# Optimization experiments

Hardware: AMD Instinct MI355X
Metric: run time of the kernel (lower is better)

The kernel has to match this reference:

```python
import jax, jax.numpy as jnp
import numpy as np
from jax import lax

B, S, E, H, V, L = 16, 256, 256, 256, 50000, 9


def setup_inputs() -> dict:
    key = jax.random.key(0)
    ks = jax.random.split(key, 12)
    s = 0.05
    return {
        "input_ids": jax.random.randint(ks[0], (B, S), 0, V),
        "attention_mask": jnp.ones((B, S), dtype=jnp.int32),
        "labels": jax.random.randint(ks[1], (B, S), 0, L),
        "embedding": jax.random.normal(ks[2], (V, E), jnp.float32) * s,
        "w_ih_l0": jax.random.normal(ks[3], (2, 4 * H, E), jnp.float32) * s,
        "w_ih_rest": jax.random.normal(ks[4], (3, 2, 4 * H, 2 * H), jnp.float32) * s,
        "w_hh": jax.random.normal(ks[5], (4, 2, 4 * H, H), jnp.float32) * s,
        "b": jax.random.normal(ks[6], (4, 2, 2, 4 * H), jnp.float32) * s,
        "ln_g": jnp.ones((2 * H,), jnp.float32),
        "ln_b": jnp.zeros((2 * H,), jnp.float32),
        "lin_w": jax.random.normal(ks[7], (L, 2 * H), jnp.float32) * s,
        "lin_b": jnp.zeros((L,), jnp.float32),
        "crf_start": jax.random.normal(ks[8], (L,), jnp.float32) * s,
        "crf_end": jax.random.normal(ks[9], (L,), jnp.float32) * s,
        "crf_trans": jax.random.normal(ks[10], (L, L), jnp.float32) * s,
    }


def _lstm_dir(x, w_ih, w_hh, b_ih, b_hh, reverse):
    # x: [B,S,in]; PyTorch gate order i,f,g,o packed along 4H.
    Bb = x.shape[0]
    Hh = w_hh.shape[1]
    xg = jnp.einsum('bsi,gi->bsg', x, w_ih) + b_ih + b_hh  # precompute input projection
    if reverse:
        xg = xg[:, ::-1]

    def step(carry, g):
        h, c = carry
        g = g + h @ w_hh.T
        i, f, gg, o = jnp.split(g, 4, axis=-1)
        c = jax.nn.sigmoid(f) * c + jax.nn.sigmoid(i) * jnp.tanh(gg)
        h = jax.nn.sigmoid(o) * jnp.tanh(c)
        return (h, c), h

    z = jnp.zeros((Bb, Hh), x.dtype)
    _, hs = lax.scan(step, (z, z), jnp.swapaxes(xg, 0, 1))
    hs = jnp.swapaxes(hs, 0, 1)  # [B,S,H]
    if reverse:
        hs = hs[:, ::-1]
    return hs


def _forward(input_ids, attention_mask, labels, embedding, w_ih_l0, w_ih_rest,
             w_hh, b, ln_g, ln_b, lin_w, lin_b, crf_start, crf_end, crf_trans):
    x = embedding[input_ids]  # [B,S,E]
    for layer in range(4):
        wf = w_ih_l0[0] if layer == 0 else w_ih_rest[layer - 1, 0]
        wb = w_ih_l0[1] if layer == 0 else w_ih_rest[layer - 1, 1]
        hf = _lstm_dir(x, wf, w_hh[layer, 0], b[layer, 0, 0], b[layer, 0, 1], False)
        hb = _lstm_dir(x, wb, w_hh[layer, 1], b[layer, 1, 0], b[layer, 1, 1], True)
        x = jnp.concatenate([hf, hb], axis=-1)  # [B,S,2H]
    # dropout is identity in eval mode
    mu = x.mean(-1, keepdims=True)
    var = ((x - mu) ** 2).mean(-1, keepdims=True)
    x = (x - mu) * lax.rsqrt(var + 1e-5) * ln_g + ln_b
    logits = jnp.einsum('bsh,lh->bsl', x, lin_w) + lin_b  # emissions [B,S,L]

    # CRF negative log-likelihood (torchcrf semantics, reduction='sum')
    Bb = logits.shape[0]
    mask_f = attention_mask.astype(logits.dtype)
    bidx = jnp.arange(Bb)
    first = labels[:, 0]
    num = crf_start[first] + logits[bidx, 0, first]
    em_t = jnp.swapaxes(logits, 0, 1)[1:]  # [S-1,B,L]
    tprev = labels[:, :-1].T
    tcur = labels[:, 1:].T
    mt = mask_f[:, 1:].T

    def num_step(s, inp):
        e, tp, tc, m = inp
        return s + (crf_trans[tp, tc] + e[bidx, tc]) * m, None

    num, _ = lax.scan(num_step, num, (em_t, tprev, tcur, mt))
    last = jnp.sum(attention_mask, axis=1).astype(jnp.int32) - 1
    num = num + crf_end[labels[bidx, last]]

    alpha = crf_start + logits[:, 0]  # [B,L]

    def den_step(a, inp):
        e, m = inp
        nxt = jax.nn.logsumexp(a[:, :, None] + crf_trans[None] + e[:, None, :], axis=1)
        return jnp.where(m[:, None] > 0, nxt, a), None

    alpha, _ = lax.scan(den_step, alpha, (em_t, mt))
    denom = jax.nn.logsumexp(alpha + crf_end, axis=-1)
    loss = -(num - denom).sum()
    return logits, loss


def reference(input_ids, attention_mask, labels, embedding, w_ih_l0, w_ih_rest,
              w_hh, b, ln_g, ln_b, lin_w, lin_b, crf_start, crf_end, crf_trans):
    return _forward(input_ids, attention_mask, labels, embedding, w_ih_l0,
                    w_ih_rest, w_hh, b, ln_g, ln_b, lin_w, lin_b,
                    crf_start, crf_end, crf_trans)
```

## Files before the change

### kernel.cpp

```cpp
#include <hip/hip_runtime.h>
#include <math.h>
#include <stdint.h>

#define BB 16
#define SS 256
#define LL 9
#define ROWS 4096
#define HP 272

typedef __attribute__((ext_vector_type(8))) short short8;
typedef __attribute__((ext_vector_type(4))) float f32x4;
typedef __attribute__((ext_vector_type(8))) int i32x8;

#define HSCALE 256.0f
#define LOG2E  1.44269504f
#define WCONST 1477.3199f
#define SCALE_ONE 0x7F7F7F7Fu
#define SCALE_IFO 0x6D6D6D6Du
#define SCALE_G   0x6E6E6E6Eu

__device__ __forceinline__ unsigned short f2bf(float f) {
  unsigned u = __float_as_uint(f);
  return (unsigned short)((u + 0x7FFF + ((u >> 16) & 1)) >> 16);
}
__device__ __forceinline__ float bf2f(unsigned short s) {
  return __uint_as_float(((unsigned)s) << 16);
}

__device__ __forceinline__ void gl2lds16(const void* g, void* l) {
  __builtin_amdgcn_global_load_lds(
      (const __attribute__((address_space(1))) void*)g,
      (__attribute__((address_space(3))) void*)l, 16, 0, 0);
}

__device__ __forceinline__ void barrier_lds_only() {
  asm volatile("s_waitcnt lgkmcnt(0)" ::: "memory");
  __builtin_amdgcn_s_barrier();
  asm volatile("" ::: "memory");
}

__global__ __launch_bounds__(256) void embed_bf16(
    const int* __restrict__ ids, const float* __restrict__ emb,
    unsigned short* __restrict__ x0) {
  int row = blockIdx.x;
  int id = ids[row];
  x0[(size_t)row * 256 + threadIdx.x] = f2bf(emb[(size_t)id * 256 + threadIdx.x]);
}

__global__ __launch_bounds__(64) void pack_whh_mx(
    const float* __restrict__ w, unsigned* __restrict__ wfrag) {
  int nb = blockIdx.x, ks2 = blockIdx.y, z = blockIdx.z;
  int lane = threadIdx.x, qq = lane >> 4, col = lane & 15;
  int g = nb >> 4;
  float csc = (g == 2) ? WCONST : -WCONST;
  const float* wp = w + (size_t)z * 1024 * 256 + (size_t)(nb * 16 + col) * 256 +
                    ks2 * 128 + qq * 32;
  unsigned* op = wfrag + (((size_t)(z * 64 + nb) * 2 + ks2) * 64 + lane) * 8;
#pragma unroll
  for (int u = 0; u < 8; ++u) {
    float v0 = wp[u * 4 + 0] * csc, v1 = wp[u * 4 + 1] * csc;
    float v2 = wp[u * 4 + 2] * csc, v3 = wp[u * 4 + 3] * csc;
    unsigned pk = __builtin_amdgcn_cvt_pk_fp8_f32(v0, v1, 0, false);
    pk = __builtin_amdgcn_cvt_pk_fp8_f32(v2, v3, pk, true);
    op[u] = pk;
  }
}

__global__ __launch_bounds__(256) void bias_perm(
    const float* __restrict__ b2, float* __restrict__ biasPF) {
  int i = blockIdx.x * 256 + threadIdx.x;
  int l = i >> 11, r = i & 2047;
  int dir = r >> 10, np = r & 1023;
  int n = ((np & 3) << 8) + (np >> 2);
  float cg = ((np & 3) == 2) ? (2.0f * LOG2E) : (-LOG2E);
  biasPF[i] = (b2[l * 4096 + dir * 2048 + n] + b2[l * 4096 + dir * 2048 + 1024 + n]) * cg;
}

__global__ __launch_bounds__(256) void prep_wih(
    const float* __restrict__ w_l0, const float* __restrict__ w_rest,
    unsigned short* __restrict__ wp, const long* __restrict__ woff_dummy) {
  int l = blockIdx.z;
  int Ksh = l ? 9 : 8;
  int K = 1 << Ksh;
  long total = (long)2 * 1024 * K;
  long idx = (long)blockIdx.x * 256 + threadIdx.x;
  if (idx >= total) return;
  int k = (int)(idx & (K - 1));
  long r = idx >> Ksh;
  int np = (int)(r & 1023), dir = (int)(r >> 10);
  int nph = ((np & 3) << 8) + (np >> 2);
  float cg = ((np & 3) == 2) ? (2.0f * LOG2E) : (-LOG2E);
  const float* src = l ? (w_rest + (size_t)(l - 1) * 2 * 1024 * 512) : w_l0;
  size_t off = l ? (524288 + (size_t)(l - 1) * 1048576) : 0;
  wp[off + idx] = f2bf(src[((size_t)dir * 1024 + nph) * K + k] * cg);
}

__global__ __launch_bounds__(512) void gemm_xg128(
    const unsigned short* __restrict__ A, int K,
    const unsigned short* __restrict__ BP,
    const float* __restrict__ biasPF,
    unsigned short* __restrict__ xgP) {
  int dir = blockIdx.z;
  int n0 = blockIdx.x * 128, m0 = blockIdx.y * 128;
  int tid = threadIdx.x;
  int wv = tid >> 6, lane = tid & 63, quad = lane >> 4, col = lane & 15;
  __shared__ unsigned short As[2][128 * 32];
  __shared__ unsigned short Bs[2][128 * 32];
  const unsigned short* Bw = BP + (size_t)dir * 1024 * K;

  int srow = lane >> 2;
  int scol = (lane & 3) * 8;
  const unsigned short* ga = A + (size_t)(m0 + wv * 16 + srow) * K + scol;
  const unsigned short* gb = Bw + (size_t)(n0 + wv * 16 + srow) * K + scol;
  int lofs = wv * 512;

  int wm = wv & 1;
  int wn = wv >> 1;
  f32x4 acc[4][2];
#pragma unroll
  for (int mt = 0; mt < 4; ++mt)
#pragma unroll
    for (int nt = 0; nt < 2; ++nt) acc[mt][nt] = (f32x4){0.f, 0.f, 0.f, 0.f};

  int nIter = K >> 5;
  gl2lds16(ga, &As[0][lofs]);
  gl2lds16(gb, &Bs[0][lofs]);
  ga += 32; gb += 32;
  __syncthreads();

  for (int it = 0; it < nIter; ++it) {
    int cb = it & 1;
    if (it + 1 < nIter) {
      gl2lds16(ga, &As[cb ^ 1][lofs]);
      gl2lds16(gb, &Bs[cb ^ 1][lofs]);
      ga += 32; gb += 32;
    }
    short8 bf0 = *(const short8*)&Bs[cb][(wn * 32 + col) * 32 + quad * 8];
    short8 bf1 = *(const short8*)&Bs[cb][(wn * 32 + 16 + col) * 32 + quad * 8];
#pragma unroll
    for (int mt = 0; mt < 4; ++mt) {
      short8 af = *(const short8*)&As[cb][(wm * 64 + mt * 16 + col) * 32 + quad * 8];
      acc[mt][0] = __builtin_amdgcn_mfma_f32_16x16x32_bf16(af, bf0, acc[mt][0], 0, 0, 0);
      acc[mt][1] = __builtin_amdgcn_mfma_f32_16x16x32_bf16(af, bf1, acc[mt][1], 0, 0, 0);
    }
    __syncthreads();
  }

#pragma unroll
  for (int nt = 0; nt < 2; ++nt) {
    int np = n0 + wn * 32 + nt * 16 + col;
    float bia = biasPF[dir * 1024 + np];
#pragma unroll
    for (int mt = 0; mt < 4; ++mt) {
#pragma unroll
      for (int r = 0; r < 4; ++r) {
        int row = m0 + wm * 64 + mt * 16 + quad * 4 + r;
        xgP[((size_t)dir * ROWS + row) * 1024 + np] = f2bf(acc[mt][nt][r] + bia);
      }
    }
  }
}

__global__ __launch_bounds__(1024, 4) void lstm_mx(
    const unsigned short* __restrict__ xgP,
    const unsigned* __restrict__ wfrag,
    unsigned short* __restrict__ xout) {
  int dir = blockIdx.x & 1;
  int bg = blockIdx.x >> 1;
  int tid = threadIdx.x;
  int wv = tid >> 6, lane = tid & 63;
  int quad = lane >> 4, col = lane & 15;

  __shared__ __align__(16) unsigned char Hfrag[2][4 * HP];

  {
    int* hz = (int*)&Hfrag[0][0];
    for (int i = tid; i < HP; i += 1024) hz[i] = 0;
  }

  i32x8 wf[4][2];
#pragma unroll
  for (int g = 0; g < 4; ++g) {
    int nb = g * 16 + wv;
#pragma unroll
    for (int ks2 = 0; ks2 < 2; ++ks2)
      wf[g][ks2] = *(const i32x8*)(wfrag +
          (((size_t)(dir * 64 + nb) * 2 + ks2) * 64 + lane) * 8);
  }

  int aoff = ((lane & 15) >> 2) * HP + (lane >> 4) * 32;

  int j = 16 * wv + col;
  int b = bg * 4 + quad;
  int pos0 = dir ? (SS - 1) : 0;
  int dstep = dir ? -1 : 1;
  const unsigned short* xq_ptr =
      xgP + ((size_t)dir * ROWS + (size_t)b * SS + pos0) * 1024 + j * 4;
  unsigned short* xo_ptr = xout + ((size_t)b * SS + pos0) * 512 + dir * 256 + j;
  int xq_d = dstep * 1024;
  int xo_d = dstep * 512;
  int hw = quad * HP + j;

  float Cp = 0.f;
  int cur = 0;
  ushort4 xq_n = *(const ushort4*)xq_ptr;
  xq_ptr += xq_d;
  __syncthreads();

  for (int t = 0; t < SS; ++t) {
    ushort4 xq = xq_n;
    xq_n = *(const ushort4*)xq_ptr;
    xq_ptr += xq_d;

    i32x8 af0 = *(const i32x8*)&Hfrag[cur][aoff];
    i32x8 af1 = *(const i32x8*)&Hfrag[cur][aoff + 128];

    f32x4 acc[4];
    acc[0] = (f32x4){bf2f(xq.x), 0.f, 0.f, 0.f};
    acc[1] = (f32x4){bf2f(xq.y), 0.f, 0.f, 0.f};
    acc[2] = (f32x4){bf2f(xq.z), 0.f, 0.f, 0.f};
    acc[3] = (f32x4){bf2f(xq.w), 0.f, 0.f, 0.f};
#pragma unroll
    for (int g = 0; g < 4; ++g) {
      unsigned sb = (g == 2) ? SCALE_G : SCALE_IFO;
      acc[g] = __builtin_amdgcn_mfma_scale_f32_16x16x128_f8f6f4(
          af0, wf[g][0], acc[g], 0, 0, 0, SCALE_ONE, 0, sb);
      acc[g] = __builtin_amdgcn_mfma_scale_f32_16x16x128_f8f6f4(
          af1, wf[g][1], acc[g], 0, 0, 0, SCALE_ONE, 0, sb);
    }

    int nxt = cur ^ 1;
    float gi = acc[0][0];
    float gf = acc[1][0];
    float gt = acc[2][0];
    float go = acc[3][0];
    float si = __builtin_amdgcn_rcpf(1.0f + __builtin_amdgcn_exp2f(gi));
    float sf = __builtin_amdgcn_rcpf(1.0f + __builtin_amdgcn_exp2f(gf));
    float so = __builtin_amdgcn_rcpf(1.0f + __builtin_amdgcn_exp2f(go));
    float rg = __builtin_amdgcn_rcpf(1.0f + __builtin_amdgcn_exp2f(gt));
    float tg2 = fmaf(-4.0f * LOG2E, rg, 2.0f * LOG2E);
    Cp = fmaf(sf, Cp, si * tg2);
    float rc = __builtin_amdgcn_rcpf(1.0f + __builtin_amdgcn_exp2f(Cp));
    float h = so * fmaf(-2.0f, rc, 1.0f);

    unsigned pk = __builtin_amdgcn_cvt_pk_fp8_f32(h * HSCALE, h * HSCALE, 0, false);
    Hfrag[nxt][hw] = (unsigned char)(pk & 0xFF);
    *xo_ptr = f2bf(h);
    xo_ptr += xo_d;

    barrier_lds_only();
    cur = nxt;
  }
}

__global__ __launch_bounds__(64) void ln_logits(
    const unsigned short* __restrict__ X, const float* __restrict__ g,
    const float* __restrict__ bt, const float* __restrict__ W,
    const float* __restrict__ lb, float* __restrict__ out) {
  int row = blockIdx.x;
  int lane = threadIdx.x;
  const unsigned short* x = X + (size_t)row * 512;
  float v[8];
  float s = 0.f, s2 = 0.f;
#pragma unroll
  for (int i = 0; i < 8; ++i) {
    v[i] = bf2f(x[lane + 64 * i]);
    s += v[i];
    s2 += v[i] * v[i];
  }
#pragma unroll
  for (int off = 32; off; off >>= 1) {
    s += __shfl_down(s, off, 64);
    s2 += __shfl_down(s2, off, 64);
  }
  s = __shfl(s, 0, 64);
  s2 = __shfl(s2, 0, 64);
  float mu = s * (1.f / 512.f);
  float var = s2 * (1.f / 512.f) - mu * mu;
  float rstd = rsqrtf(var + 1e-5f);
  float y[8];
#pragma unroll
  for (int i = 0; i < 8; ++i) {
    int e = lane + 64 * i;
    y[i] = (v[i] - mu) * rstd * g[e] + bt[e];
  }
  for (int l = 0; l < LL; ++l) {
    float p = 0.f;
#pragma unroll
    for (int i = 0; i < 8; ++i) p += y[i] * W[(size_t)l * 512 + lane + 64 * i];
#pragma unroll
    for (int off = 32; off; off >>= 1) p += __shfl_down(p, off, 64);
    if (lane == 0) out[(size_t)row * LL + l] = p + lb[l];
  }
}

__global__ __launch_bounds__(256) void crf_kernel(
    const float* __restrict__ logits, const int* __restrict__ labels,
    const int* __restrict__ mask, const float* __restrict__ cs,
    const float* __restrict__ ce, const float* __restrict__ ct,
    float* __restrict__ loss_out) {
  __shared__ float trans[9][12];
  __shared__ float alpha[2][BB][12];
  __shared__ float numsh[BB];
  __shared__ float res[BB];
  int tid = threadIdx.x;
  int b = tid >> 4;
  int i = tid & 15;
  if (tid < 81) trans[tid / 9][tid % 9] = ct[tid];
  __syncthreads();
  const float* lg = logits + (size_t)b * SS * LL;
  const int* lbp = labels + (size_t)b * SS;
  const int* mk = mask + (size_t)b * SS;

  float np = 0.f;
  int msum = 0;
  for (int t = i; t < SS; t += 16) {
    msum += mk[t];
    if (t == 0) {
      int l0 = lbp[0];
      np += cs[l0] + lg[l0];
    } else {
      float m = (float)mk[t];
      np += (trans[lbp[t - 1]][lbp[t]] + lg[(size_t)t * LL + lbp[t]]) * m;
    }
  }
#pragma unroll
  for (int off = 8; off; off >>= 1) {
    np += __shfl_down(np, off, 16);
    msum += __shfl_down(msum, off, 16);
  }
  if (i == 0) {
    int last = msum - 1;
    numsh[b] = np + ce[lbp[last]];
  }

  if (i < LL) alpha[0][b][i] = cs[i] + lg[i];
  int cur = 0;
  for (int t = 1; t < SS; ++t) {
    if (i < LL) {
      float e = lg[(size_t)t * LL + i];
      float av[9];
      float mmax = -1e30f;
#pragma unroll
      for (int p = 0; p < LL; ++p) {
        float vv = alpha[cur][b][p] + trans[p][i];
        av[p] = vv;
        mmax = fmaxf(mmax, vv);
      }
      float ssum = 0.f;
#pragma unroll
      for (int p = 0; p < LL; ++p) ssum += __expf(av[p] - mmax);
      float anew = e + mmax + logf(ssum);
      float aold = alpha[cur][b][i];
      alpha[cur ^ 1][b][i] = (mk[t] > 0) ? anew : aold;
    }
    cur ^= 1;
  }
  if (i == 0) {
    float arr[9];
    float m2 = -1e30f;
#pragma unroll
    for (int cc = 0; cc < LL; ++cc) {
      arr[cc] = alpha[cur][b][cc] + ce[cc];
      m2 = fmaxf(m2, arr[cc]);
    }
    float ssd = 0.f;
#pragma unroll
    for (int cc = 0; cc < LL; ++cc) ssd += __expf(arr[cc] - m2);
    float denom = m2 + logf(ssd);
    res[b] = numsh[b] - denom;
  }
  __syncthreads();
  if (tid == 0) {
    float Lsum = 0.f;
    for (int b2 = 0; b2 < BB; ++b2) Lsum += res[b2];
    loss_out[0] = -Lsum;
  }
}

extern "C" void kernel_launch(void* const* d_in, const int* in_sizes, int n_in,
                              void* d_out, int out_size, void* d_ws, size_t ws_size,
                              hipStream_t stream) {
  const int* input_ids = (const int*)d_in[0];
  const int* attn_mask = (const int*)d_in[1];
  const int* labels = (const int*)d_in[2];
  const float* embedding = (const float*)d_in[3];
  const float* w_ih_l0 = (const float*)d_in[4];
  const float* w_ih_rest = (const float*)d_in[5];
  const float* w_hh = (const float*)d_in[6];
  const float* bvec = (const float*)d_in[7];
  const float* ln_g = (const float*)d_in[8];
  const float* ln_b = (const float*)d_in[9];
  const float* lin_w = (const float*)d_in[10];
  const float* lin_b = (const float*)d_in[11];
  const float* crf_start = (const float*)d_in[12];
  const float* crf_end = (const float*)d_in[13];
  const float* crf_trans = (const float*)d_in[14];
  float* out = (float*)d_out;
  char* base = (char*)d_ws;

  unsigned short* x0    = (unsigned short*)(base);
  unsigned short* xoutA = (unsigned short*)(base + (2u << 20));
  unsigned short* xoutB = (unsigned short*)(base + (6u << 20));
  unsigned short* xgP   = (unsigned short*)(base + (10u << 20));
  unsigned*       wfrag = (unsigned*)(base + (26u << 20));
  float*          biasPF= (float*)(base + (28u << 20));
  unsigned short* wihP  = (unsigned short*)(base + (29u << 20));

  embed_bf16<<<ROWS, 256, 0, stream>>>(input_ids, embedding, x0);
  pack_whh_mx<<<dim3(64, 2, 8), 64, 0, stream>>>(w_hh, wfrag);
  bias_perm<<<32, 256, 0, stream>>>(bvec, biasPF);
  prep_wih<<<dim3(4096, 1, 4), 256, 0, stream>>>(w_ih_l0, w_ih_rest, wihP, nullptr);

  const size_t WOFF[4] = {0, 524288, 1572864, 2621440};

  const unsigned short* cur = x0;
  unsigned short* nxt = xoutA;
  for (int l = 0; l < 4; ++l) {
    int K = l ? 512 : 256;
    gemm_xg128<<<dim3(8, 32, 2), 512, 0, stream>>>(
        cur, K, wihP + WOFF[l], biasPF + (size_t)l * 2048, xgP);
    lstm_mx<<<8, 1024, 0, stream>>>(xgP, wfrag + (size_t)l * 131072, nxt);
    cur = nxt;
    nxt = (nxt == xoutA) ? xoutB : xoutA;
  }

  ln_logits<<<ROWS, 64, 0, stream>>>(cur, ln_g, ln_b, lin_w, lin_b, out);
  crf_kernel<<<1, 256, 0, stream>>>(out, labels, attn_mask, crf_start, crf_end,
                                    crf_trans, out + (size_t)ROWS * LL);
}
```

Before: 1.001 ms.

## Fuse prep kernels, stage GEMM epilogue through LDS, pack LN rows per block

Merges the four preprocessing kernels (embedding gather, W_ih pack, W_hh fp8 pack, bias permute) into one launch dispatched by block index, which removes three kernel launches. The xg GEMM epilogue now writes its tile into LDS and stores it to global memory as coalesced 16-byte vectors, replacing the scattered 2-byte stores. ln_logits handles four rows per 256-thread block instead of one row per 64-thread block. Total time is dominated by the sequential LSTM kernels, so these changes only trim launch and memory overhead around them.

```diff
diff --git a/kernel.cpp b/kernel.cpp
--- a/kernel.cpp
+++ b/kernel.cpp
@@ -39,60 +39,74 @@
   asm volatile("" ::: "memory");
 }
 
-__global__ __launch_bounds__(256) void embed_bf16(
+__global__ __launch_bounds__(256) void prep_all(
     const int* __restrict__ ids, const float* __restrict__ emb,
-    unsigned short* __restrict__ x0) {
-  int row = blockIdx.x;
-  int id = ids[row];
-  x0[(size_t)row * 256 + threadIdx.x] = f2bf(emb[(size_t)id * 256 + threadIdx.x]);
-}
-
-__global__ __launch_bounds__(64) void pack_whh_mx(
-    const float* __restrict__ w, unsigned* __restrict__ wfrag) {
-  int nb = blockIdx.x, ks2 = blockIdx.y, z = blockIdx.z;
-  int lane = threadIdx.x, qq = lane >> 4, col = lane & 15;
-  int g = nb >> 4;
-  float csc = (g == 2) ? WCONST : -WCONST;
-  const float* wp = w + (size_t)z * 1024 * 256 + (size_t)(nb * 16 + col) * 256 +
-                    ks2 * 128 + qq * 32;
-  unsigned* op = wfrag + (((size_t)(z * 64 + nb) * 2 + ks2) * 64 + lane) * 8;
-#pragma unroll
-  for (int u = 0; u < 8; ++u) {
-    float v0 = wp[u * 4 + 0] * csc, v1 = wp[u * 4 + 1] * csc;
-    float v2 = wp[u * 4 + 2] * csc, v3 = wp[u * 4 + 3] * csc;
-    unsigned pk = __builtin_amdgcn_cvt_pk_fp8_f32(v0, v1, 0, false);
-    pk = __builtin_amdgcn_cvt_pk_fp8_f32(v2, v3, pk, true);
-    op[u] = pk;
-  }
-}
-
-__global__ __launch_bounds__(256) void bias_perm(
+    unsigned short* __restrict__ x0,
+    const float* __restrict__ w_l0, const float* __restrict__ w_rest,
+    unsigned short* __restrict__ wp,
+    const float* __restrict__ whh, unsigned* __restrict__ wfrag,
     const float* __restrict__ b2, float* __restrict__ biasPF) {
-  int i = blockIdx.x * 256 + threadIdx.x;
+  int bid = blockIdx.x;
+  int tid = threadIdx.x;
+
+  if (bid < 4096) {
+    int id = ids[bid];
+    x0[(size_t)bid * 256 + tid] = f2bf(emb[(size_t)id * 256 + tid]);
+    return;
+  }
+  bid -= 4096;
+
+  if (bid < 16384) {
+    int l = bid >> 12;
+    int bx = bid & 4095;
+    int Ksh = l ? 9 : 8;
+    int K = 1 << Ksh;
+    long total = (long)2 * 1024 * K;
+    long idx = (long)bx * 256 + tid;
+    if (idx >= total) return;
+    int k = (int)(idx & (K - 1));
+    long r = idx >> Ksh;
+    int np = (int)(r & 1023), dir = (int)(r >> 10);
+    int nph = ((np & 3) << 8) + (np >> 2);
+    float cg = ((np & 3) == 2) ? (2.0f * LOG2E) : (-LOG2E);
+    const float* src = l ? (w_rest + (size_t)(l - 1) * 2 * 1024 * 512) : w_l0;
+    size_t off = l ? (524288 + (size_t)(l - 1) * 1048576) : 0;
+    wp[off + idx] = f2bf(src[((size_t)dir * 1024 + nph) * K + k] * cg);
+    return;
+  }
+  bid -= 16384;
+
+  if (bid < 256) {
+    int u = bid * 4 + (tid >> 6);
+    int lane = tid & 63;
+    int z = u >> 7;
+    int rr = u & 127;
+    int ks2 = rr >> 6;
+    int nb = rr & 63;
+    int qq = lane >> 4, col = lane & 15;
+    int g = nb >> 4;
+    float csc = (g == 2) ? WCONST : -WCONST;
+    const float* wpp = whh + (size_t)z * 1024 * 256 +
+                       (size_t)(nb * 16 + col) * 256 + ks2 * 128 + qq * 32;
+    unsigned* op = wfrag + (((size_t)(z * 64 + nb) * 2 + ks2) * 64 + lane) * 8;
+#pragma unroll
+    for (int uu = 0; uu < 8; ++uu) {
+      float v0 = wpp[uu * 4 + 0] * csc, v1 = wpp[uu * 4 + 1] * csc;
+      float v2 = wpp[uu * 4 + 2] * csc, v3 = wpp[uu * 4 + 3] * csc;
+      unsigned pk = __builtin_amdgcn_cvt_pk_fp8_f32(v0, v1, 0, false);
+      pk = __builtin_amdgcn_cvt_pk_fp8_f32(v2, v3, pk, true);
+      op[uu] = pk;
+    }
+    return;
+  }
+  bid -= 256;
+
+  int i = bid * 256 + tid;
   int l = i >> 11, r = i & 2047;
   int dir = r >> 10, np = r & 1023;
   int n = ((np & 3) << 8) + (np >> 2);
   float cg = ((np & 3) == 2) ? (2.0f * LOG2E) : (-LOG2E);
   biasPF[i] = (b2[l * 4096 + dir * 2048 + n] + b2[l * 4096 + dir * 2048 + 1024 + n]) * cg;
-}
-
-__global__ __launch_bounds__(256) void prep_wih(
-    const float* __restrict__ w_l0, const float* __restrict__ w_rest,
-    unsigned short* __restrict__ wp, const long* __restrict__ woff_dummy) {
-  int l = blockIdx.z;
-  int Ksh = l ? 9 : 8;
-  int K = 1 << Ksh;
-  long total = (long)2 * 1024 * K;
-  long idx = (long)blockIdx.x * 256 + threadIdx.x;
-  if (idx >= total) return;
-  int k = (int)(idx & (K - 1));
-  long r = idx >> Ksh;
-  int np = (int)(r & 1023), dir = (int)(r >> 10);
-  int nph = ((np & 3) << 8) + (np >> 2);
-  float cg = ((np & 3) == 2) ? (2.0f * LOG2E) : (-LOG2E);
-  const float* src = l ? (w_rest + (size_t)(l - 1) * 2 * 1024 * 512) : w_l0;
-  size_t off = l ? (524288 + (size_t)(l - 1) * 1048576) : 0;
-  wp[off + idx] = f2bf(src[((size_t)dir * 1024 + nph) * K + k] * cg);
 }
 
 __global__ __launch_bounds__(512) void gemm_xg128(
@@ -104,8 +118,7 @@
   int n0 = blockIdx.x * 128, m0 = blockIdx.y * 128;
   int tid = threadIdx.x;
   int wv = tid >> 6, lane = tid & 63, quad = lane >> 4, col = lane & 15;
-  __shared__ unsigned short As[2][128 * 32];
-  __shared__ unsigned short Bs[2][128 * 32];
+  __shared__ unsigned short Ls[16384];
   const unsigned short* Bw = BP + (size_t)dir * 1024 * K;
 
   int srow = lane >> 2;
@@ -123,23 +136,25 @@
     for (int nt = 0; nt < 2; ++nt) acc[mt][nt] = (f32x4){0.f, 0.f, 0.f, 0.f};
 
   int nIter = K >> 5;
-  gl2lds16(ga, &As[0][lofs]);
-  gl2lds16(gb, &Bs[0][lofs]);
+  gl2lds16(ga, &Ls[lofs]);
+  gl2lds16(gb, &Ls[8192 + lofs]);
   ga += 32; gb += 32;
   __syncthreads();
 
   for (int it = 0; it < nIter; ++it) {
     int cb = it & 1;
     if (it + 1 < nIter) {
-      gl2lds16(ga, &As[cb ^ 1][lofs]);
-      gl2lds16(gb, &Bs[cb ^ 1][lofs]);
+      gl2lds16(ga, &Ls[(cb ^ 1) * 4096 + lofs]);
+      gl2lds16(gb, &Ls[8192 + (cb ^ 1) * 4096 + lofs]);
       ga += 32; gb += 32;
     }
-    short8 bf0 = *(const short8*)&Bs[cb][(wn * 32 + col) * 32 + quad * 8];
-    short8 bf1 = *(const short8*)&Bs[cb][(wn * 32 + 16 + col) * 32 + quad * 8];
+    const unsigned short* Ab = &Ls[cb * 4096];
+    const unsigned short* Bb = &Ls[8192 + cb * 4096];
+    short8 bf0 = *(const short8*)&Bb[(wn * 32 + col) * 32 + quad * 8];
+    short8 bf1 = *(const short8*)&Bb[(wn * 32 + 16 + col) * 32 + quad * 8];
 #pragma unroll
     for (int mt = 0; mt < 4; ++mt) {
-      short8 af = *(const short8*)&As[cb][(wm * 64 + mt * 16 + col) * 32 + quad * 8];
+      short8 af = *(const short8*)&Ab[(wm * 64 + mt * 16 + col) * 32 + quad * 8];
       acc[mt][0] = __builtin_amdgcn_mfma_f32_16x16x32_bf16(af, bf0, acc[mt][0], 0, 0, 0);
       acc[mt][1] = __builtin_amdgcn_mfma_f32_16x16x32_bf16(af, bf1, acc[mt][1], 0, 0, 0);
     }
@@ -148,16 +163,22 @@
 
 #pragma unroll
   for (int nt = 0; nt < 2; ++nt) {
-    int np = n0 + wn * 32 + nt * 16 + col;
-    float bia = biasPF[dir * 1024 + np];
-#pragma unroll
-    for (int mt = 0; mt < 4; ++mt) {
-#pragma unroll
-      for (int r = 0; r < 4; ++r) {
-        int row = m0 + wm * 64 + mt * 16 + quad * 4 + r;
-        xgP[((size_t)dir * ROWS + row) * 1024 + np] = f2bf(acc[mt][nt][r] + bia);
-      }
-    }
+    int npl = wn * 32 + nt * 16 + col;
+    float bia = biasPF[dir * 1024 + n0 + npl];
+#pragma unroll
+    for (int mt = 0; mt < 4; ++mt)
+#pragma unroll
+      for (int r = 0; r < 4; ++r)
+        Ls[(wm * 64 + mt * 16 + quad * 4 + r) * 128 + npl] =
+            f2bf(acc[mt][nt][r] + bia);
+  }
+  __syncthreads();
+  unsigned short* od = xgP + (size_t)dir * ROWS * 1024;
+#pragma unroll
+  for (int it = 0; it < 4; ++it) {
+    int e = (it * 512 + tid) * 8;
+    int row = e >> 7, npl = e & 127;
+    *(short8*)&od[(size_t)(m0 + row) * 1024 + n0 + npl] = *(const short8*)&Ls[e];
   }
 }
 
@@ -253,12 +274,12 @@
   }
 }
 
-__global__ __launch_bounds__(64) void ln_logits(
+__global__ __launch_bounds__(256) void ln_logits(
     const unsigned short* __restrict__ X, const float* __restrict__ g,
     const float* __restrict__ bt, const float* __restrict__ W,
     const float* __restrict__ lb, float* __restrict__ out) {
-  int row = blockIdx.x;
-  int lane = threadIdx.x;
+  int row = blockIdx.x * 4 + (threadIdx.x >> 6);
+  int lane = threadIdx.x & 63;
   const unsigned short* x = X + (size_t)row * 512;
   float v[8];
   float s = 0.f, s2 = 0.f;
@@ -407,10 +428,9 @@
   float*          biasPF= (float*)(base + (28u << 20));
   unsigned short* wihP  = (unsigned short*)(base + (29u << 20));
 
-  embed_bf16<<<ROWS, 256, 0, stream>>>(input_ids, embedding, x0);
-  pack_whh_mx<<<dim3(64, 2, 8), 64, 0, stream>>>(w_hh, wfrag);
-  bias_perm<<<32, 256, 0, stream>>>(bvec, biasPF);
-  prep_wih<<<dim3(4096, 1, 4), 256, 0, stream>>>(w_ih_l0, w_ih_rest, wihP, nullptr);
+  prep_all<<<20768, 256, 0, stream>>>(input_ids, embedding, x0,
+                                      w_ih_l0, w_ih_rest, wihP,
+                                      w_hh, wfrag, bvec, biasPF);
 
   const size_t WOFF[4] = {0, 524288, 1572864, 2621440};
 
@@ -425,7 +445,7 @@
     nxt = (nxt == xoutA) ? xoutB : xoutA;
   }
 
-  ln_logits<<<ROWS, 64, 0, stream>>>(cur, ln_g, ln_b, lin_w, lin_b, out);
+  ln_logits<<<1024, 256, 0, stream>>>(cur, ln_g, ln_b, lin_w, lin_b, out);
   crf_kernel<<<1, 256, 0, stream>>>(out, labels, attn_mask, crf_start, crf_end,
                                     crf_trans, out + (size_t)ROWS * LL);
 }
```

Measured after the change: 993.2 us. No clear change (-0.7%).
